# Kernel optimization log

Measured on AMD Instinct MI355X. Metric: run time of the kernel, lower is better.

The kernel has to match this reference:

```python
import jax, jax.numpy as jnp
import numpy as np

BS, C, D_IN, D_OUT, H = 64, 512, 256, 256, 4
HD = D_OUT // H


def setup_inputs() -> dict:
    key = jax.random.key(0)
    ks = jax.random.split(key, 8)
    def xavier(k, shape):
        fan_in, fan_out = shape[-1], shape[-2] if len(shape) > 1 else shape[-1]
        lim = float(np.sqrt(6.0 / (fan_in + fan_out)))
        return jax.random.uniform(k, shape, jnp.float32, -lim, lim)
    return {
        "h": jax.random.normal(ks[0], (BS, C, D_IN), jnp.float32),
        "A_fc": jax.random.uniform(ks[1], (BS, C, C), jnp.float32),
        "W": xavier(ks[2], (D_OUT, D_IN)),            # Linear(in_dim,out_dim,bias=False).weight
        "a": xavier(ks[3], (H, 2 * HD)),               # attention vector per head
        "W1": xavier(ks[4], (64, D_OUT)),              # channel_agg Linear(out_dim,64)
        "b1": jnp.zeros((64,), jnp.float32),
        "W2": xavier(ks[5], (1, 64)),                  # channel_agg Linear(64,1)
        "b2": jnp.zeros((1,), jnp.float32),
    }


def reference(h, A_fc, W, a, W1, b1, W2, b2):
    bs, c, _ = h.shape
    heads, hd = a.shape[0], a.shape[1] // 2
    # Wh: [BS, C, H, hd]
    Wh = (h @ W.T).reshape(bs, c, heads, hd)
    # a . cat(Wh_i, Wh_j) decomposes into two small projections broadcast-added
    e_i = jnp.einsum('nchd,hd->nch', Wh, a[:, :hd])   # varies over node i
    e_j = jnp.einsum('nchd,hd->nch', Wh, a[:, hd:])   # varies over node j
    e = e_i[:, :, None, :] + e_j[:, None, :, :]        # [BS, Ci, Cj, H]
    e = jax.nn.leaky_relu(e, negative_slope=0.2)
    e = jnp.transpose(e, (0, 3, 1, 2))                 # [BS, H, C, C]
    # prior-weighted scores, softmax over neighbors j (dropout = identity in eval)
    attn = jax.nn.softmax(e * A_fc[:, None, :, :], axis=-1)
    # aggregate: [BS,H,C,C] @ [BS,H,C,hd] -> [BS,C,H,hd] -> [BS,C,out_dim]
    h_prime = jnp.einsum('nhij,njhd->nihd', attn, Wh).reshape(bs, c, heads * hd)
    # channel gating MLP + softmax over channel dim
    s = jnp.tanh(h_prime @ W1.T + b1) @ W2.T + b2      # [BS, C, 1]
    w = jax.nn.softmax(s, axis=1)
    return jnp.sum(h_prime * w, axis=1)                # [BS, out_dim]
```

## Files before the change

kernel.cpp:

```cpp
#include <hip/hip_runtime.h>
#include <hip/hip_bf16.h>

#define BS 64
#define C 512
#define DIN 256
#define DOUT 256
#define H 4
#define HD 64

typedef __attribute__((ext_vector_type(8))) short short8;
typedef __attribute__((ext_vector_type(4))) short short4v;
typedef __attribute__((ext_vector_type(4))) float f32x4;

__device__ __forceinline__ short bfc(float f) {
    union { __hip_bfloat16 h; unsigned short s; } u;
    u.h = __float2bfloat16(f);
    return (short)u.s;
}

__device__ __forceinline__ float bf2f(short v) {
    union { unsigned u; float f; } x;
    x.u = ((unsigned)(unsigned short)v) << 16;
    return x.f;
}

__device__ __forceinline__ short8 pack8n(const float* p) {
    short8 r;
#pragma unroll
    for (int i = 0; i < 8; ++i) r[i] = bfc(p[i]);
    return r;
}

__global__ __launch_bounds__(256) void k0_prep(
    const float* __restrict__ W, const float* __restrict__ W1,
    short* __restrict__ Wbf, short* __restrict__ W1bf)
{
    const int idx = blockIdx.x * 256 + threadIdx.x;
    if (idx < 8192) {
        float t[8];
        *(float4*)(t)     = *(const float4*)(W + idx * 8);
        *(float4*)(t + 4) = *(const float4*)(W + idx * 8 + 4);
        *(short8*)(Wbf + idx * 8) = pack8n(t);
    } else if (idx < 10240) {
        const int j = idx - 8192;
        float t[8];
        *(float4*)(t)     = *(const float4*)(W1 + j * 8);
        *(float4*)(t + 4) = *(const float4*)(W1 + j * 8 + 4);
        *(short8*)(W1bf + j * 8) = pack8n(t);
    }
}

__global__ __launch_bounds__(256) void k1_gemm(
    const float* __restrict__ hsrc, const short* __restrict__ Wbf,
    const float* __restrict__ avec,
    short* __restrict__ whT, float* __restrict__ ei, float* __restrict__ ej)
{
    __shared__ __align__(16) short hs[64 * 256];
    const int tid = threadIdx.x;
    const int l = tid & 63;
    const int w = tid >> 6;
    const int lr = l & 15;
    const int g = l >> 4;
    const int kg = g * 8;
    const int mtile = blockIdx.x;
    const int row0 = mtile * 64;
    const float L2E = 1.44269504088896f;

#pragma unroll
    for (int it = 0; it < 8; ++it) {
        const int idx = tid + it * 256;
        const int row = idx >> 5;
        const int colg = idx & 31;
        const float* p = hsrc + (size_t)(row0 + row) * DIN + colg * 8;
        float t[8];
        *(float4*)(t)     = *(const float4*)(p);
        *(float4*)(t + 4) = *(const float4*)(p + 4);
        const int off = (row * 512 + colg * 16) ^ ((row & 7) << 4);
        *(short8*)((char*)hs + off) = pack8n(t);
    }
    __syncthreads();

    const int head = w;
    f32x4 acc[4][4];
#pragma unroll
    for (int i = 0; i < 4; ++i)
#pragma unroll
        for (int j = 0; j < 4; ++j) acc[i][j] = f32x4{0.f, 0.f, 0.f, 0.f};

    for (int k0 = 0; k0 < DIN; k0 += 32) {
        short8 af[4];
#pragma unroll
        for (int rt = 0; rt < 4; ++rt) {
            const int row = rt * 16 + lr;
            const int off = (row * 512 + (k0 + kg) * 2) ^ ((row & 7) << 4);
            af[rt] = *(const short8*)((const char*)hs + off);
        }
        short8 bfr[4];
#pragma unroll
        for (int ct = 0; ct < 4; ++ct)
            bfr[ct] = *(const short8*)(Wbf + (size_t)(head * 64 + ct * 16 + lr) * DIN + k0 + kg);
#pragma unroll
        for (int rt = 0; rt < 4; ++rt)
#pragma unroll
            for (int ct = 0; ct < 4; ++ct)
                acc[rt][ct] = __builtin_amdgcn_mfma_f32_16x16x32_bf16(
                    af[rt], bfr[ct], acc[rt][ct], 0, 0, 0);
    }

    float avi[4], avj[4];
#pragma unroll
    for (int ct = 0; ct < 4; ++ct) {
        avi[ct] = avec[head * 2 * HD + ct * 16 + lr];
        avj[ct] = avec[head * 2 * HD + HD + ct * 16 + lr];
    }

    const int jt = mtile & 7;
    const int bb = mtile >> 3;
    short* fragb = whT + (size_t)(bb * H + head) * (HD * C);

#pragma unroll
    for (int rt = 0; rt < 4; ++rt) {
        const int lane2 = lr + 16 * ((rt & 1) * 2 + (g >> 1));
        const int t0 = (g & 1) * 4;
        const int half = rt >> 1;
#pragma unroll
        for (int ct = 0; ct < 4; ++ct) {
            short4v sv;
#pragma unroll
            for (int reg = 0; reg < 4; ++reg) sv[reg] = bfc(acc[rt][ct][reg]);
            *(short4v*)(fragb + (jt * 4 + ct) * 1024 + half * 512 + lane2 * 8 + t0) = sv;
        }
#pragma unroll
        for (int reg = 0; reg < 4; ++reg) {
            const int j = row0 + rt * 16 + g * 4 + reg;
            const int b = j >> 9;
            const int c = j & 511;
            float pi = 0.f, pj = 0.f;
#pragma unroll
            for (int ct = 0; ct < 4; ++ct) {
                pi += acc[rt][ct][reg] * avi[ct];
                pj += acc[rt][ct][reg] * avj[ct];
            }
#pragma unroll
            for (int off = 1; off < 16; off <<= 1) {
                pi += __shfl_xor(pi, off);
                pj += __shfl_xor(pj, off);
            }
            if (lr == 0) {
                ei[(b * H + head) * C + c] = pi * L2E;
                ej[(b * H + head) * C + c] = pj * L2E;
            }
        }
    }
}

__global__ __launch_bounds__(256) void k2_attn(
    const float* __restrict__ Afc, const short* __restrict__ whT,
    const float* __restrict__ ei, const float* __restrict__ ej,
    short* __restrict__ hpb)
{
    __shared__ __align__(16) short alds[16 * 520];
    const int tid = threadIdx.x;
    const int l = tid & 63;
    const int hh = tid >> 6;
    const int swz = (blockIdx.x & 7) * 256 + (blockIdx.x >> 3);
    const int b = swz >> 5;
    const int i0 = (swz & 31) * 16;
    const int lr = l & 15;
    const int kg = (l >> 4) * 8;

    {
        const float* asrc = Afc + ((size_t)b * C + i0) * C;
#pragma unroll
        for (int k = 0; k < 4; ++k) {
            const int idx = tid + k * 256;
            const int row = idx >> 6;
            const int colg = idx & 63;
            const float* p = asrc + row * 512 + colg * 8;
            float t[8];
            *(float4*)(t)     = *(const float4*)(p);
            *(float4*)(t + 4) = *(const float4*)(p + 4);
            *(short8*)(alds + row * 520 + colg * 8) = pack8n(t);
        }
    }
    __syncthreads();

    f32x4 O[4];
#pragma unroll
    for (int dt = 0; dt < 4; ++dt) O[dt] = f32x4{0.f, 0.f, 0.f, 0.f};
    float ls0 = 0.f, ls1 = 0.f, ls2 = 0.f, ls3 = 0.f;

    const float eiv = ei[(b * H + hh) * C + i0 + lr];
    const float* ejb = ej + (b * H + hh) * C;
    const short* vb = whT + (size_t)(b * H + hh) * (HD * C);
    const short* arowp = alds + lr * 520;

    for (int jt = 0; jt < 8; ++jt) {
        const int j0 = jt * 64;

        short8 vf[4][2];
#pragma unroll
        for (int dt = 0; dt < 4; ++dt) {
            const short* vp = vb + (jt * 4 + dt) * 1024 + l * 8;
            vf[dt][0] = *(const short8*)(vp);
            vf[dt][1] = *(const short8*)(vp + 512);
        }

        float ejv[16];
        *(float4*)(ejv)      = *(const float4*)(ejb + j0 + kg);
        *(float4*)(ejv + 4)  = *(const float4*)(ejb + j0 + kg + 4);
        *(float4*)(ejv + 8)  = *(const float4*)(ejb + j0 + 32 + kg);
        *(float4*)(ejv + 12) = *(const float4*)(ejb + j0 + 32 + kg + 4);

        union { short8 s; unsigned u[4]; } a0, a1;
        a0.s = *(const short8*)(arowp + j0 + kg);
        a1.s = *(const short8*)(arowp + j0 + 32 + kg);
        float av[16];
#pragma unroll
        for (int i = 0; i < 4; ++i) {
            union { unsigned u; float f; } lo, hi;
            lo.u = a0.u[i] << 16;
            hi.u = a0.u[i] & 0xffff0000u;
            av[2 * i]     = lo.f;
            av[2 * i + 1] = hi.f;
            lo.u = a1.u[i] << 16;
            hi.u = a1.u[i] & 0xffff0000u;
            av[8 + 2 * i]     = lo.f;
            av[8 + 2 * i + 1] = hi.f;
        }

#pragma unroll
        for (int t = 0; t < 16; ++t) {
            const float z = eiv + ejv[t];
            const float zl = fmaxf(z, 0.2f * z);
            const float e = exp2f(zl * av[t]);
            av[t] = e;
            if ((t & 3) == 0) ls0 += e;
            else if ((t & 3) == 1) ls1 += e;
            else if ((t & 3) == 2) ls2 += e;
            else ls3 += e;
        }

        const short8 pa0 = pack8n(av);
        const short8 pa1 = pack8n(av + 8);
#pragma unroll
        for (int dt = 0; dt < 4; ++dt) {
            O[dt] = __builtin_amdgcn_mfma_f32_16x16x32_bf16(pa0, vf[dt][0], O[dt], 0, 0, 0);
            O[dt] = __builtin_amdgcn_mfma_f32_16x16x32_bf16(pa1, vf[dt][1], O[dt], 0, 0, 0);
        }
    }

    float lsum = (ls0 + ls1) + (ls2 + ls3);
    lsum += __shfl_xor(lsum, 16);
    lsum += __shfl_xor(lsum, 32);
    const float inv = 1.0f / lsum;
    float fr[4];
#pragma unroll
    for (int reg = 0; reg < 4; ++reg)
        fr[reg] = __shfl(inv, (l >> 4) * 4 + reg);
#pragma unroll
    for (int dt = 0; dt < 4; ++dt)
#pragma unroll
        for (int reg = 0; reg < 4; ++reg) {
            const int c = i0 + (l >> 4) * 4 + reg;
            hpb[((size_t)b * C + c) * DOUT + hh * HD + dt * 16 + lr] =
                bfc(O[dt][reg] * fr[reg]);
        }
}

__global__ __launch_bounds__(256) void k3_gate(
    const short* __restrict__ hpb, const short* __restrict__ W1bf,
    const float* __restrict__ b1, const float* __restrict__ W2,
    const float* __restrict__ b2, float* __restrict__ sgate)
{
    __shared__ __align__(16) short hs[64 * 256];
    const int t = threadIdx.x;
    const int l = t & 63;
    const int w = t >> 6;
    const int b = blockIdx.x >> 3;
    const int c0 = (blockIdx.x & 7) * 64;
    const int lr = l & 15;
    const int kg = (l >> 4) * 8;

    {
        const short* src = hpb + ((size_t)b * C + c0) * DOUT;
#pragma unroll
        for (int it = 0; it < 8; ++it) {
            const int idx = t + it * 256;
            const int row = idx >> 5;
            const int colg = idx & 31;
            const int off = (row * 512 + colg * 16) ^ ((row & 7) << 4);
            *(short8*)((char*)hs + off) = *(const short8*)(src + row * 256 + colg * 8);
        }
    }
    __syncthreads();

    f32x4 acc[4];
#pragma unroll
    for (int ct = 0; ct < 4; ++ct) acc[ct] = f32x4{0.f, 0.f, 0.f, 0.f};

    const int myrow = w * 16 + lr;
    for (int k0 = 0; k0 < DOUT; k0 += 32) {
        const int off = (myrow * 512 + (k0 + kg) * 2) ^ ((myrow & 7) << 4);
        const short8 af = *(const short8*)((const char*)hs + off);
#pragma unroll
        for (int ct = 0; ct < 4; ++ct) {
            const short8 bfr = *(const short8*)(W1bf + (size_t)(ct * 16 + lr) * DOUT + k0 + kg);
            acc[ct] = __builtin_amdgcn_mfma_f32_16x16x32_bf16(af, bfr, acc[ct], 0, 0, 0);
        }
    }

    float b1v[4], w2v[4];
#pragma unroll
    for (int ct = 0; ct < 4; ++ct) {
        b1v[ct] = b1[ct * 16 + lr];
        w2v[ct] = W2[ct * 16 + lr];
    }
    const float b2v = b2[0];
#pragma unroll
    for (int reg = 0; reg < 4; ++reg) {
        float val = 0.f;
#pragma unroll
        for (int ct = 0; ct < 4; ++ct)
            val += tanhf(acc[ct][reg] + b1v[ct]) * w2v[ct];
#pragma unroll
        for (int off = 1; off < 16; off <<= 1) val += __shfl_xor(val, off);
        if (lr == 0)
            sgate[b * C + c0 + w * 16 + (l >> 4) * 4 + reg] = val + b2v;
    }
}

__global__ __launch_bounds__(256) void k4a_partial(
    const short* __restrict__ hpb, const float* __restrict__ sgate,
    float* __restrict__ partial)
{
    __shared__ float red[16];
    __shared__ float wlds[64];
    const int t = threadIdx.x;
    const int b = blockIdx.x >> 3;
    const int c0 = (blockIdx.x & 7) * 64;
    const int l = t & 63, w = t >> 6;
    const float L2E = 1.44269504088896f;

    const float s0 = sgate[b * C + t], s1 = sgate[b * C + 256 + t];
    float mx = fmaxf(s0, s1);
#pragma unroll
    for (int off = 1; off < 64; off <<= 1) mx = fmaxf(mx, __shfl_xor(mx, off));
    if (l == 0) red[w] = mx;
    __syncthreads();
    mx = fmaxf(fmaxf(red[0], red[1]), fmaxf(red[2], red[3]));
    float sum = exp2f((s0 - mx) * L2E) + exp2f((s1 - mx) * L2E);
#pragma unroll
    for (int off = 1; off < 64; off <<= 1) sum += __shfl_xor(sum, off);
    if (l == 0) red[8 + w] = sum;
    __syncthreads();
    sum = red[8] + red[9] + red[10] + red[11];
    const float inv = 1.f / sum;
    if (t < 64)
        wlds[t] = exp2f((sgate[b * C + c0 + t] - mx) * L2E) * inv;
    __syncthreads();

    float acc = 0.f;
    const short* base = hpb + ((size_t)b * C + c0) * DOUT + t;
#pragma unroll 4
    for (int c = 0; c < 64; ++c) acc += wlds[c] * bf2f(base[(size_t)c * DOUT]);
    partial[(size_t)blockIdx.x * DOUT + t] = acc;
}

__global__ __launch_bounds__(256) void k4b_reduce(
    const float* __restrict__ partial, float* __restrict__ out)
{
    const int t = threadIdx.x;
    const int b = blockIdx.x;
    float s = 0.f;
#pragma unroll
    for (int k = 0; k < 8; ++k)
        s += partial[(size_t)(b * 8 + k) * DOUT + t];
    out[b * DOUT + t] = s;
}

extern "C" void kernel_launch(void* const* d_in, const int* in_sizes, int n_in,
                              void* d_out, int out_size, void* d_ws, size_t ws_size,
                              hipStream_t stream) {
    const float* hsrc = (const float*)d_in[0];
    const float* Afc  = (const float*)d_in[1];
    const float* W    = (const float*)d_in[2];
    const float* avec = (const float*)d_in[3];
    const float* W1   = (const float*)d_in[4];
    const float* b1   = (const float*)d_in[5];
    const float* W2   = (const float*)d_in[6];
    const float* b2   = (const float*)d_in[7];

    char* ws = (char*)d_ws;
    short* whT   = (short*)(ws);
    float* ei    = (float*)(ws + 16777216);
    float* ej    = (float*)(ws + 17301504);
    short* hpb   = (short*)(ws + 17825792);
    float* sg    = (float*)(ws + 34603008);
    float* parts = (float*)(ws + 34734080);
    short* Wbf   = (short*)(ws + 35258368);
    short* W1bf  = (short*)(ws + 35389440);

    hipLaunchKernelGGL(k0_prep, dim3(40), dim3(256), 0, stream, W, W1, Wbf, W1bf);
    hipLaunchKernelGGL(k1_gemm, dim3(512), dim3(256), 0, stream, hsrc, Wbf, avec, whT, ei, ej);
    hipLaunchKernelGGL(k2_attn, dim3(2048), dim3(256), 0, stream, Afc, whT, ei, ej, hpb);
    hipLaunchKernelGGL(k3_gate, dim3(512), dim3(256), 0, stream, hpb, W1bf, b1, W2, b2, sg);
    hipLaunchKernelGGL(k4a_partial, dim3(512), dim3(256), 0, stream, hpb, sg, parts);
    hipLaunchKernelGGL(k4b_reduce, dim3(64), dim3(256), 0, stream, parts, (float*)d_out);
}
```

Before: 83.31 us.

## Process two 16-row query tiles per attention block to reuse V fragments

Each k2_attn block now covers 32 rows of i instead of 16, so every wave computes two sets of 16x16 MFMA accumulators that share the same loaded V (whT) fragments and ej values. Grid size drops from 2048 to 1024 blocks and the LDS buffer for A_fc rows doubles. The aim is to halve global traffic for V and ej per output row and give more independent MFMA chains. The cost is higher register pressure and LDS use per block, which may lower occupancy.

```diff
diff --git a/kernel.cpp b/kernel.cpp
--- a/kernel.cpp
+++ b/kernel.cpp
@@ -159,20 +159,20 @@
     const float* __restrict__ ei, const float* __restrict__ ej,
     short* __restrict__ hpb)
 {
-    __shared__ __align__(16) short alds[16 * 520];
+    __shared__ __align__(16) short alds[32 * 520];
     const int tid = threadIdx.x;
     const int l = tid & 63;
     const int hh = tid >> 6;
-    const int swz = (blockIdx.x & 7) * 256 + (blockIdx.x >> 3);
-    const int b = swz >> 5;
-    const int i0 = (swz & 31) * 16;
+    const int swz = (blockIdx.x & 7) * 128 + (blockIdx.x >> 3);
+    const int b = swz >> 4;
+    const int i0 = (swz & 15) * 32;
     const int lr = l & 15;
     const int kg = (l >> 4) * 8;
 
     {
         const float* asrc = Afc + ((size_t)b * C + i0) * C;
 #pragma unroll
-        for (int k = 0; k < 4; ++k) {
+        for (int k = 0; k < 8; ++k) {
             const int idx = tid + k * 256;
             const int row = idx >> 6;
             const int colg = idx & 63;
@@ -185,15 +185,20 @@
     }
     __syncthreads();
 
-    f32x4 O[4];
-#pragma unroll
-    for (int dt = 0; dt < 4; ++dt) O[dt] = f32x4{0.f, 0.f, 0.f, 0.f};
-    float ls0 = 0.f, ls1 = 0.f, ls2 = 0.f, ls3 = 0.f;
-
-    const float eiv = ei[(b * H + hh) * C + i0 + lr];
+    f32x4 O0[4], O1[4];
+#pragma unroll
+    for (int dt = 0; dt < 4; ++dt) {
+        O0[dt] = f32x4{0.f, 0.f, 0.f, 0.f};
+        O1[dt] = f32x4{0.f, 0.f, 0.f, 0.f};
+    }
+    float lsa0 = 0.f, lsb0 = 0.f, lsa1 = 0.f, lsb1 = 0.f;
+
+    const float eiv0 = ei[(b * H + hh) * C + i0 + lr];
+    const float eiv1 = ei[(b * H + hh) * C + i0 + 16 + lr];
     const float* ejb = ej + (b * H + hh) * C;
     const short* vb = whT + (size_t)(b * H + hh) * (HD * C);
-    const short* arowp = alds + lr * 520;
+    const short* arow0 = alds + lr * 520;
+    const short* arow1 = alds + (16 + lr) * 520;
 
     for (int jt = 0; jt < 8; ++jt) {
         const int j0 = jt * 64;
@@ -212,59 +217,76 @@
         *(float4*)(ejv + 8)  = *(const float4*)(ejb + j0 + 32 + kg);
         *(float4*)(ejv + 12) = *(const float4*)(ejb + j0 + 32 + kg + 4);
 
-        union { short8 s; unsigned u[4]; } a0, a1;
-        a0.s = *(const short8*)(arowp + j0 + kg);
-        a1.s = *(const short8*)(arowp + j0 + 32 + kg);
-        float av[16];
+        union { short8 s; unsigned u[4]; } a00, a01, a10, a11;
+        a00.s = *(const short8*)(arow0 + j0 + kg);
+        a01.s = *(const short8*)(arow0 + j0 + 32 + kg);
+        a10.s = *(const short8*)(arow1 + j0 + kg);
+        a11.s = *(const short8*)(arow1 + j0 + 32 + kg);
+
+        float av0[16], av1[16];
 #pragma unroll
         for (int i = 0; i < 4; ++i) {
-            union { unsigned u; float f; } lo, hi;
-            lo.u = a0.u[i] << 16;
-            hi.u = a0.u[i] & 0xffff0000u;
-            av[2 * i]     = lo.f;
-            av[2 * i + 1] = hi.f;
-            lo.u = a1.u[i] << 16;
-            hi.u = a1.u[i] & 0xffff0000u;
-            av[8 + 2 * i]     = lo.f;
-            av[8 + 2 * i + 1] = hi.f;
+            union { unsigned u; float f; } x;
+            x.u = a00.u[i] << 16;        av0[2 * i] = x.f;
+            x.u = a00.u[i] & 0xffff0000u; av0[2 * i + 1] = x.f;
+            x.u = a01.u[i] << 16;        av0[8 + 2 * i] = x.f;
+            x.u = a01.u[i] & 0xffff0000u; av0[8 + 2 * i + 1] = x.f;
+            x.u = a10.u[i] << 16;        av1[2 * i] = x.f;
+            x.u = a10.u[i] & 0xffff0000u; av1[2 * i + 1] = x.f;
+            x.u = a11.u[i] << 16;        av1[8 + 2 * i] = x.f;
+            x.u = a11.u[i] & 0xffff0000u; av1[8 + 2 * i + 1] = x.f;
         }
 
 #pragma unroll
         for (int t = 0; t < 16; ++t) {
-            const float z = eiv + ejv[t];
-            const float zl = fmaxf(z, 0.2f * z);
-            const float e = exp2f(zl * av[t]);
-            av[t] = e;
-            if ((t & 3) == 0) ls0 += e;
-            else if ((t & 3) == 1) ls1 += e;
-            else if ((t & 3) == 2) ls2 += e;
-            else ls3 += e;
-        }
-
-        const short8 pa0 = pack8n(av);
-        const short8 pa1 = pack8n(av + 8);
+            const float z0 = eiv0 + ejv[t];
+            const float z1 = eiv1 + ejv[t];
+            const float zl0 = fmaxf(z0, 0.2f * z0);
+            const float zl1 = fmaxf(z1, 0.2f * z1);
+            const float e0 = exp2f(zl0 * av0[t]);
+            const float e1 = exp2f(zl1 * av1[t]);
+            av0[t] = e0;
+            av1[t] = e1;
+            if (t & 1) { lsb0 += e0; lsb1 += e1; }
+            else       { lsa0 += e0; lsa1 += e1; }
+        }
+
+        const short8 p00 = pack8n(av0);
+        const short8 p01 = pack8n(av0 + 8);
+        const short8 p10 = pack8n(av1);
+        const short8 p11 = pack8n(av1 + 8);
 #pragma unroll
         for (int dt = 0; dt < 4; ++dt) {
-            O[dt] = __builtin_amdgcn_mfma_f32_16x16x32_bf16(pa0, vf[dt][0], O[dt], 0, 0, 0);
-            O[dt] = __builtin_amdgcn_mfma_f32_16x16x32_bf16(pa1, vf[dt][1], O[dt], 0, 0, 0);
-        }
-    }
-
-    float lsum = (ls0 + ls1) + (ls2 + ls3);
-    lsum += __shfl_xor(lsum, 16);
-    lsum += __shfl_xor(lsum, 32);
-    const float inv = 1.0f / lsum;
-    float fr[4];
-#pragma unroll
-    for (int reg = 0; reg < 4; ++reg)
-        fr[reg] = __shfl(inv, (l >> 4) * 4 + reg);
+            O0[dt] = __builtin_amdgcn_mfma_f32_16x16x32_bf16(p00, vf[dt][0], O0[dt], 0, 0, 0);
+            O1[dt] = __builtin_amdgcn_mfma_f32_16x16x32_bf16(p10, vf[dt][0], O1[dt], 0, 0, 0);
+            O0[dt] = __builtin_amdgcn_mfma_f32_16x16x32_bf16(p01, vf[dt][1], O0[dt], 0, 0, 0);
+            O1[dt] = __builtin_amdgcn_mfma_f32_16x16x32_bf16(p11, vf[dt][1], O1[dt], 0, 0, 0);
+        }
+    }
+
+    float lsum0 = lsa0 + lsb0;
+    float lsum1 = lsa1 + lsb1;
+    lsum0 += __shfl_xor(lsum0, 16);
+    lsum0 += __shfl_xor(lsum0, 32);
+    lsum1 += __shfl_xor(lsum1, 16);
+    lsum1 += __shfl_xor(lsum1, 32);
+    const float inv0 = 1.0f / lsum0;
+    const float inv1 = 1.0f / lsum1;
+    float fr0[4], fr1[4];
+#pragma unroll
+    for (int reg = 0; reg < 4; ++reg) {
+        fr0[reg] = __shfl(inv0, (l >> 4) * 4 + reg);
+        fr1[reg] = __shfl(inv1, (l >> 4) * 4 + reg);
+    }
 #pragma unroll
     for (int dt = 0; dt < 4; ++dt)
 #pragma unroll
         for (int reg = 0; reg < 4; ++reg) {
-            const int c = i0 + (l >> 4) * 4 + reg;
-            hpb[((size_t)b * C + c) * DOUT + hh * HD + dt * 16 + lr] =
-                bfc(O[dt][reg] * fr[reg]);
+            const int c0 = i0 + (l >> 4) * 4 + reg;
+            hpb[((size_t)b * C + c0) * DOUT + hh * HD + dt * 16 + lr] =
+                bfc(O0[dt][reg] * fr0[reg]);
+            hpb[((size_t)b * C + c0 + 16) * DOUT + hh * HD + dt * 16 + lr] =
+                bfc(O1[dt][reg] * fr1[reg]);
         }
 }
 
@@ -403,7 +425,7 @@
 
     hipLaunchKernelGGL(k0_prep, dim3(40), dim3(256), 0, stream, W, W1, Wbf, W1bf);
     hipLaunchKernelGGL(k1_gemm, dim3(512), dim3(256), 0, stream, hsrc, Wbf, avec, whT, ei, ej);
-    hipLaunchKernelGGL(k2_attn, dim3(2048), dim3(256), 0, stream, Afc, whT, ei, ej, hpb);
+    hipLaunchKernelGGL(k2_attn, dim3(1024), dim3(256), 0, stream, Afc, whT, ei, ej, hpb);
     hipLaunchKernelGGL(k3_gate, dim3(512), dim3(256), 0, stream, hpb, W1bf, b1, W2, b2, sg);
     hipLaunchKernelGGL(k4a_partial, dim3(512), dim3(256), 0, stream, hpb, sg, parts);
     hipLaunchKernelGGL(k4b_reduce, dim3(64), dim3(256), 0, stream, parts, (float*)d_out);
```

Measured after the change: 83.37 us. About the same (+0.1%).
